# Optimization experiments

Hardware: AMD Instinct MI355X
Metric: run time of the kernel (lower is better)

## Reference

```python
import jax, jax.numpy as jnp
import numpy as np

N_NODES = 32768
N_EDGES = 524288
NODE_DIM, POS_DIM, EDGE_DIM = 44, 8, 1
HID, OUT, LAYERS, HEADS = 128, 128, 3, 4
DK = HID // HEADS
LN_EPS = 1e-5


def _linear_w(key, fan_in, fan_out):
    return (jax.random.normal(key, (fan_in, fan_out), jnp.float32) / np.sqrt(fan_in)).astype(jnp.float32)


def _ln(x, g, b):
    m = jnp.mean(x, axis=-1, keepdims=True)
    v = jnp.var(x, axis=-1, keepdims=True)
    return (x - m) * jax.lax.rsqrt(v + LN_EPS) * g + b


def setup_inputs() -> dict:
    key = jax.random.key(0)
    ks = jax.random.split(key, 16)
    inp = {
        'feats': jax.random.normal(ks[0], (N_NODES, NODE_DIM), jnp.float32),
        'lap_pos_enc': jax.random.normal(ks[1], (N_NODES, POS_DIM), jnp.float32),
        'edge_feats': jax.random.normal(ks[2], (N_EDGES, EDGE_DIM), jnp.float32),
        'src': jax.random.randint(ks[3], (N_EDGES,), 0, N_NODES, jnp.int32),
        'dst': jax.random.randint(ks[4], (N_EDGES,), 0, N_NODES, jnp.int32),
        # input projections
        'W_node': _linear_w(ks[5], NODE_DIM, HID), 'b_node': jnp.zeros((HID,), jnp.float32),
        'W_pos': _linear_w(ks[6], POS_DIM, HID), 'b_pos': jnp.zeros((HID,), jnp.float32),
        'W_edge': _linear_w(ks[7], EDGE_DIM, HID), 'b_edge': jnp.zeros((HID,), jnp.float32),
    }
    # per-layer stacked params (all layers are HID->HID since OUT==HID)
    def stack(k, fi, fo):
        kk = jax.random.split(k, LAYERS)
        return jnp.stack([_linear_w(kk[i], fi, fo) for i in range(LAYERS)])
    inp['Wq'] = stack(ks[8], HID, HID)
    inp['Wk'] = stack(ks[9], HID, HID)
    inp['Wv'] = stack(ks[10], HID, HID)
    inp['We'] = stack(ks[11], HID, HID)
    inp['W_lin'] = stack(ks[12], HID, HID)
    inp['b_lin'] = jnp.zeros((LAYERS, HID), jnp.float32)
    inp['g1'] = jnp.ones((LAYERS, HID), jnp.float32)
    inp['be1'] = jnp.zeros((LAYERS, HID), jnp.float32)
    inp['Wf1'] = stack(ks[13], HID, 2 * HID)
    inp['bf1'] = jnp.zeros((LAYERS, 2 * HID), jnp.float32)
    inp['Wf2'] = stack(ks[14], 2 * HID, HID)
    inp['bf2'] = jnp.zeros((LAYERS, HID), jnp.float32)
    inp['g2'] = jnp.ones((LAYERS, HID), jnp.float32)
    inp['be2'] = jnp.zeros((LAYERS, HID), jnp.float32)
    return inp


def reference(feats, lap_pos_enc, edge_feats,
              W_node, b_node, W_pos, b_pos, W_edge, b_edge,
              Wq, Wk, Wv, We, W_lin, b_lin, g1, be1,
              Wf1, bf1, Wf2, bf2, g2, be2, src, dst):
    n = feats.shape[0]
    inv_sqrt_dk = np.float32(1.0 / np.sqrt(DK))
    h = feats @ W_node + b_node + lap_pos_enc @ W_pos + b_pos      # [N, HID]
    e = edge_feats @ W_edge + b_edge                               # [E, HID] (shared across layers)
    for i in range(LAYERS):
        Q = (h @ Wq[i]).reshape(n, HEADS, DK)
        K = (h @ Wk[i]).reshape(n, HEADS, DK)
        V = (h @ Wv[i]).reshape(n, HEADS, DK)
        E = (e @ We[i]).reshape(-1, HEADS, DK)                     # [E, H, DK]
        # raw score [E, H, 1] broadcast against (1+E) -> [E, H, DK] (faithful to source)
        score = jnp.sum(K[src] * Q[dst], axis=-1, keepdims=True) * inv_sqrt_dk
        score = score * (1.0 + E)
        alpha = jnp.exp(score)                                      # [E, H, DK]
        Z = jnp.maximum(jax.ops.segment_sum(alpha, dst, num_segments=n), 1e-6)
        h_out = jax.ops.segment_sum(V[src] * alpha, dst, num_segments=n) / Z
        h_out = h_out.reshape(n, HEADS * DK)
        h = h + h_out @ W_lin[i] + b_lin[i]                        # residual + dropout(identity)
        h = _ln(h, g1[i], be1[i])
        h2 = jax.nn.relu(h @ Wf1[i] + bf1[i]) @ Wf2[i] + bf2[i]
        h = _ln(h + h2, g2[i], be2[i])
    # dgl.mean_nodes over a single graph -> [1, OUT]; readout LayerNorm is never applied in source
    return jnp.mean(h, axis=0, keepdims=True)
```

## Files before the change

kernel.cpp:

```cpp
#include <hip/hip_runtime.h>
#include <hip/hip_bf16.h>

#define N_NODES 32768
#define N_EDGES 524288
#define LN_EPS 1e-5f

typedef unsigned short ushort_t;
typedef __attribute__((ext_vector_type(8))) short short8v;
typedef __attribute__((ext_vector_type(4))) float float4v;
typedef __attribute__((ext_vector_type(2))) float float2v;

__device__ __forceinline__ float bf2f(ushort_t u) {
    return __uint_as_float(((unsigned int)u) << 16);
}
__device__ __forceinline__ ushort_t f2bf(float f) {
    unsigned int u = __float_as_uint(f);
    unsigned int r = (u + 0x7FFFu + ((u >> 16) & 1u)) >> 16;
    return (ushort_t)r;
}
__device__ __forceinline__ float lo16(unsigned int x) { return __uint_as_float(x << 16); }
__device__ __forceinline__ float hi16(unsigned int x) { return __uint_as_float(x & 0xFFFF0000u); }

#if __has_builtin(__builtin_amdgcn_exp2f)
#define EXP2(x) __builtin_amdgcn_exp2f(x)
#else
#define EXP2(x) exp2f(x)
#endif

#define OFF_WNODE 0
#define OFF_BNODE 5632
#define OFF_WPOS  5760
#define OFF_BPOS  6784
#define OFF_WEDGE 6912
#define OFF_BEDGE 7040
#define OFF_WQ    7168
#define OFF_WK    56320
#define OFF_WV    105472
#define OFF_WE    154624
#define OFF_WLIN  203776
#define OFF_BLIN  252928
#define OFF_G1    253312
#define OFF_BE1   253696
#define OFF_WF1   254080
#define OFF_BF1   352384
#define OFF_WF2   353152
#define OFF_BF2   451456
#define OFF_G2    451840
#define OFF_BE2   452224
#define CONV_TOTAL 452608

#define REC_QKV(i)  ((i) * 96)
#define REC_WLIN(i) (288 + (i) * 32)
#define REC_WF1(i)  (384 + (i) * 64)
#define REC_WF2(i)  (576 + (i) * 64)
#define REC_TOTAL   768

#define LDS_STRIDE 264
#define LDS_FSTRIDE 132

__global__ void detect_kernel(const unsigned int* __restrict__ wn, int* __restrict__ flag) {
    __shared__ int s[256];
    int t = threadIdx.x;
    int cnt = 0;
    for (int i = t; i < 2816; i += 256) {
        unsigned int b = (wn[i] >> 8) & 0x7F;
        cnt += (b >= 0x3A && b <= 0x40) ? 1 : 0;
    }
    s[t] = cnt;
    __syncthreads();
    for (int off = 128; off > 0; off >>= 1) {
        if (t < off) s[t] += s[t + off];
        __syncthreads();
    }
    if (t == 0) *flag = (s[0] > 1408) ? 1 : 0;
}

struct ConvArgs { const void* src[20]; };

__global__ void convert_kernel(ConvArgs a, const int* __restrict__ flag,
                               float* __restrict__ dst) {
    int gid = blockIdx.x * 256 + threadIdx.x;
    if (gid >= CONV_TOTAL) return;
    const int off[21] = {OFF_WNODE, OFF_BNODE, OFF_WPOS, OFF_BPOS, OFF_WEDGE, OFF_BEDGE,
                         OFF_WQ, OFF_WK, OFF_WV, OFF_WE, OFF_WLIN, OFF_BLIN, OFF_G1,
                         OFF_BE1, OFF_WF1, OFF_BF1, OFF_WF2, OFF_BF2, OFF_G2, OFF_BE2,
                         CONV_TOTAL};
    int s = 0;
#pragma unroll
    for (int i = 1; i < 20; ++i) s += (gid >= off[i]) ? 1 : 0;
    int local = gid - off[s];
    if (*flag)
        dst[gid] = bf2f(((const ushort_t*)a.src[s])[local]);
    else
        dst[gid] = ((const float*)a.src[s])[local];
}

__global__ void swz_kernel(const float* __restrict__ conv, ushort_t* __restrict__ swz) {
    int gid = blockIdx.x * 256 + threadIdx.x;
    int lane = gid & 63;
    int rec = gid >> 6;
    if (rec >= REC_TOTAL) return;
    int col = lane & 15, quad = lane >> 4;
    const float* src;
    int ct, kb, OC;
    if (rec < 288) {
        int layer = rec / 96, r2 = rec % 96;
        ct = r2 >> 2; kb = r2 & 3;
        int seg = ct >> 3;
        int base = (seg == 0 ? OFF_WQ : (seg == 1 ? OFF_WK : OFF_WV)) + layer * 16384;
        src = conv + base; OC = 128; ct &= 7;
    } else if (rec < 384) {
        int r = rec - 288, layer = r / 32, r2 = r % 32;
        ct = r2 >> 2; kb = r2 & 3;
        src = conv + OFF_WLIN + layer * 16384; OC = 128;
    } else if (rec < 576) {
        int r = rec - 384, layer = r / 64, r2 = r % 64;
        ct = r2 >> 2; kb = r2 & 3;
        src = conv + OFF_WF1 + layer * 32768; OC = 256;
    } else {
        int r = rec - 576, layer = r / 64, r2 = r % 64;
        ct = r2 >> 3; kb = r2 & 7;
        src = conv + OFF_WF2 + layer * 32768; OC = 128;
    }
    int n = ct * 16 + col;
    ushort_t v[8];
#pragma unroll
    for (int j = 0; j < 8; ++j) v[j] = f2bf(src[(size_t)(kb * 32 + quad * 8 + j) * OC + n]);
    ushort_t* o = swz + (size_t)rec * 512 + lane * 8;
#pragma unroll
    for (int j = 0; j < 8; ++j) o[j] = v[j];
}

__global__ void input_proj_kernel(const void* __restrict__ feats,
                                  const void* __restrict__ lap,
                                  const float* __restrict__ conv,
                                  const int* __restrict__ flag,
                                  float* __restrict__ h, ushort_t* __restrict__ hb) {
    int gid = blockIdx.x * 256 + threadIdx.x;
    int node = gid >> 5;
    int cg = (gid & 31) * 4;
    bool isbf = (*flag != 0);
    const float* Wn = conv + OFF_WNODE;
    const float* Wp = conv + OFF_WPOS;

    float4 b1 = *(const float4*)(conv + OFF_BNODE + cg);
    float4 b2 = *(const float4*)(conv + OFF_BPOS + cg);
    float a0 = b1.x + b2.x, a1 = b1.y + b2.y, a2 = b1.z + b2.z, a3 = b1.w + b2.w;

#define ACC(fv, Wbase, kk)                                            \
    {                                                                 \
        float4 wv_ = *(const float4*)(Wbase + (size_t)(kk) * 128 + cg); \
        a0 = fmaf(fv, wv_.x, a0);                                     \
        a1 = fmaf(fv, wv_.y, a1);                                     \
        a2 = fmaf(fv, wv_.z, a2);                                     \
        a3 = fmaf(fv, wv_.w, a3);                                     \
    }

    if (isbf) {
        const ushort_t* frow = (const ushort_t*)feats + (size_t)node * 44;
        const ushort_t* prow = (const ushort_t*)lap + (size_t)node * 8;
#pragma unroll
        for (int i = 0; i < 11; ++i) {
            ushort4 f = *(const ushort4*)(frow + i * 4);
            ACC(bf2f(f.x), Wn, i * 4 + 0)
            ACC(bf2f(f.y), Wn, i * 4 + 1)
            ACC(bf2f(f.z), Wn, i * 4 + 2)
            ACC(bf2f(f.w), Wn, i * 4 + 3)
        }
#pragma unroll
        for (int i = 0; i < 2; ++i) {
            ushort4 f = *(const ushort4*)(prow + i * 4);
            ACC(bf2f(f.x), Wp, i * 4 + 0)
            ACC(bf2f(f.y), Wp, i * 4 + 1)
            ACC(bf2f(f.z), Wp, i * 4 + 2)
            ACC(bf2f(f.w), Wp, i * 4 + 3)
        }
    } else {
        const float4* frow = (const float4*)((const float*)feats + (size_t)node * 44);
        const float4* prow = (const float4*)((const float*)lap + (size_t)node * 8);
#pragma unroll
        for (int i = 0; i < 11; ++i) {
            float4 f = frow[i];
            ACC(f.x, Wn, i * 4 + 0)
            ACC(f.y, Wn, i * 4 + 1)
            ACC(f.z, Wn, i * 4 + 2)
            ACC(f.w, Wn, i * 4 + 3)
        }
#pragma unroll
        for (int i = 0; i < 2; ++i) {
            float4 f = prow[i];
            ACC(f.x, Wp, i * 4 + 0)
            ACC(f.y, Wp, i * 4 + 1)
            ACC(f.z, Wp, i * 4 + 2)
            ACC(f.w, Wp, i * 4 + 3)
        }
    }
#undef ACC

    size_t idx = (size_t)node * 128 + cg;
    *(float4*)(h + idx) = make_float4(a0, a1, a2, a3);
    ushort4 ob;
    ob.x = f2bf(a0); ob.y = f2bf(a1); ob.z = f2bf(a2); ob.w = f2bf(a3);
    *(ushort4*)(hb + idx) = ob;
}

__global__ void uc_kernel(const float* __restrict__ conv,
                          float* __restrict__ u, float* __restrict__ c1) {
    int l = blockIdx.x;
    int d = threadIdx.x;
    const float* W_edge = conv + OFF_WEDGE;
    const float* b_edge = conv + OFF_BEDGE;
    const float* Wl = conv + OFF_WE + l * 128 * 128;
    float uu = 0.f, cc = 0.f;
#pragma unroll 4
    for (int k = 0; k < 128; ++k) {
        float w = Wl[k * 128 + d];
        uu += W_edge[k] * w;
        cc += b_edge[k] * w;
    }
    const float scale = 0.17677669529663687f * 1.4426950408889634f;
    u[l * 128 + d] = uu * scale;
    c1[l * 128 + d] = (1.f + cc) * scale;
}

__global__ void hist_kernel(const int* __restrict__ dst, int* __restrict__ deg) {
    int e = blockIdx.x * 256 + threadIdx.x;
    if (e < N_EDGES) atomicAdd(&deg[dst[e]], 1);
}

__global__ void scan_kernel(const int* __restrict__ deg, int* __restrict__ rowstart,
                            int* __restrict__ cursor) {
    __shared__ int lds[1024];
    int t = threadIdx.x;
    int base = t * 32;
    int v[32];
    int csum = 0;
#pragma unroll
    for (int j = 0; j < 32; ++j) { v[j] = deg[base + j]; csum += v[j]; }
    lds[t] = csum;
    __syncthreads();
    for (int off = 1; off < 1024; off <<= 1) {
        int x = (t >= off) ? lds[t - off] : 0;
        __syncthreads();
        lds[t] += x;
        __syncthreads();
    }
    int excl = lds[t] - csum;
    int running = excl;
#pragma unroll
    for (int j = 0; j < 32; ++j) {
        rowstart[base + j] = running;
        cursor[base + j] = running;
        running += v[j];
    }
    if (t == 1023) rowstart[N_NODES] = running;
}

__global__ void scatter_kernel(const int* __restrict__ src, const int* __restrict__ dst,
                               const void* __restrict__ ef, const int* __restrict__ flag,
                               int* __restrict__ cursor,
                               unsigned int* __restrict__ edges) {
    int e = blockIdx.x * 256 + threadIdx.x;
    if (e < N_EDGES) {
        ushort_t efb = (*flag != 0) ? ((const ushort_t*)ef)[e]
                                    : f2bf(((const float*)ef)[e]);
        int d = dst[e];
        int p = atomicAdd(&cursor[d], 1);
        edges[p] = (unsigned int)src[e] | ((unsigned int)efb << 16);
    }
}

template <int KB>
__global__ __launch_bounds__(256) void qkv_gemm(
    const ushort_t* __restrict__ A,
    const ushort_t* __restrict__ Bswz,
    ushort_t* __restrict__ outQ,
    unsigned char* __restrict__ outKV) {
    const int K = KB * 32;
    const int tid = threadIdx.x;
    const int wv = tid >> 6, lane = tid & 63;
    const int col = lane & 15, quad = lane >> 4;
    const int m0 = blockIdx.x * 64 + wv * 16;
    const int ct0 = blockIdx.y * 8;

    float4v acc[8];
#pragma unroll
    for (int ct = 0; ct < 8; ++ct) acc[ct] = (float4v){0.f, 0.f, 0.f, 0.f};

    const ushort_t* Ap = A + (size_t)(m0 + col) * K + quad * 8;
    const ushort_t* Bp = Bswz + (size_t)ct0 * KB * 512 + lane * 8;

#pragma unroll
    for (int kb = 0; kb < KB; ++kb) {
        short8v a = *(const short8v*)(Ap + kb * 32);
#pragma unroll
        for (int ct = 0; ct < 8; ++ct) {
            short8v b = *(const short8v*)(Bp + (size_t)(ct * KB + kb) * 512);
            acc[ct] = __builtin_amdgcn_mfma_f32_16x16x32_bf16(a, b, acc[ct], 0, 0, 0);
        }
    }

    const int rowb = m0 + quad * 4;
    const int seg = blockIdx.y;
    if (seg == 0) {
#pragma unroll
        for (int ct = 0; ct < 8; ++ct) {
            int j = ct * 16 + col;
#pragma unroll
            for (int r = 0; r < 4; ++r)
                outQ[(size_t)(rowb + r) * 128 + j] = f2bf(acc[ct][r]);
        }
    } else {
        const int vofs = (seg == 2) ? 8 : 0;
#pragma unroll
        for (int ct = 0; ct < 8; ++ct) {
            int j = ct * 16 + col;
            int off = ((j >> 3) * 16) + (j & 7) + vofs;
#pragma unroll
            for (int r = 0; r < 4; ++r) {
                float a = acc[ct][r];
                float b = __shfl_xor(a, 1, 64);
                if ((col & 1) == 0) {
                    unsigned short pk = (unsigned short)
                        __builtin_amdgcn_cvt_pk_fp8_f32(a, b, 0, false);
                    *(ushort_t*)(outKV + (size_t)(rowb + r) * 256 + off) = pk;
                }
            }
        }
    }
}

__global__ __launch_bounds__(64, 2) void ffn_kernel(
    const ushort_t* __restrict__ HOUT,
    const ushort_t* __restrict__ BWL,
    const ushort_t* __restrict__ BF1,
    const ushort_t* __restrict__ BF2,
    const float* __restrict__ bl,
    const float* __restrict__ g1v, const float* __restrict__ be1v,
    const float* __restrict__ bf1v,
    const float* __restrict__ bf2v,
    const float* __restrict__ g2v, const float* __restrict__ be2v,
    float* __restrict__ h,
    ushort_t* __restrict__ hb) {
    __shared__ __align__(16) char ldsraw[16 * 528];
    ushort_t* ldsu = (ushort_t*)ldsraw;
    float* ldsf = (float*)ldsraw;
    const int lane = threadIdx.x & 63;
    const int col = lane & 15, quad = lane >> 4;
    const int m0 = blockIdx.x * 16;
    const int rowb = m0 + quad * 4;
    const int lrowc = quad * 4;
    const int lrowa = col;

    float4v acc[8];
#pragma unroll
    for (int ct = 0; ct < 8; ++ct) acc[ct] = (float4v){0.f, 0.f, 0.f, 0.f};
    const ushort_t* Ap = HOUT + (size_t)(m0 + col) * 128 + quad * 8;
#pragma unroll
    for (int kb = 0; kb < 4; ++kb) {
        short8v a = *(const short8v*)(Ap + kb * 32);
#pragma unroll
        for (int ct = 0; ct < 8; ++ct) {
            short8v b = *(const short8v*)(BWL + (size_t)(ct * 4 + kb) * 512 + lane * 8);
            acc[ct] = __builtin_amdgcn_mfma_f32_16x16x32_bf16(a, b, acc[ct], 0, 0, 0);
        }
    }

    float val[8][4], s[4] = {0.f, 0.f, 0.f, 0.f}, ss[4] = {0.f, 0.f, 0.f, 0.f};
#pragma unroll
    for (int ct = 0; ct < 8; ++ct) {
        float bi = bl[ct * 16 + col];
#pragma unroll
        for (int r = 0; r < 4; ++r) {
            float v = acc[ct][r] + bi + h[(size_t)(rowb + r) * 128 + ct * 16 + col];
            val[ct][r] = v;
            s[r] += v;
            ss[r] += v * v;
        }
    }
#pragma unroll
    for (int mask = 1; mask < 16; mask <<= 1) {
#pragma unroll
        for (int r = 0; r < 4; ++r) {
            s[r] += __shfl_xor(s[r], mask, 64);
            ss[r] += __shfl_xor(ss[r], mask, 64);
        }
    }
#pragma unroll
    for (int r = 0; r < 4; ++r) {
        float mean = s[r] * (1.f / 128.f);
        float var = ss[r] * (1.f / 128.f) - mean * mean;
        s[r] = mean;
        ss[r] = rsqrtf(var + LN_EPS);
    }
#pragma unroll
    for (int ct = 0; ct < 8; ++ct) {
        float gg = g1v[ct * 16 + col], bb = be1v[ct * 16 + col];
#pragma unroll
        for (int r = 0; r < 4; ++r) {
            float o = (val[ct][r] - s[r]) * ss[r] * gg + bb;
            val[ct][r] = o;
            ldsu[(lrowc + r) * LDS_STRIDE + ct * 16 + col] = f2bf(o);
        }
    }
    __syncthreads();

    short8v af[4];
#pragma unroll
    for (int kb = 0; kb < 4; ++kb)
        af[kb] = *(const short8v*)&ldsu[lrowa * LDS_STRIDE + kb * 32 + quad * 8];

    float4v acc2[16];
#pragma unroll
    for (int ct = 0; ct < 16; ++ct) acc2[ct] = (float4v){0.f, 0.f, 0.f, 0.f};
#pragma unroll
    for (int kb = 0; kb < 4; ++kb) {
#pragma unroll
        for (int ct = 0; ct < 16; ++ct) {
            short8v b = *(const short8v*)(BF1 + (size_t)(ct * 4 + kb) * 512 + lane * 8);
            acc2[ct] = __builtin_amdgcn_mfma_f32_16x16x32_bf16(af[kb], b, acc2[ct], 0, 0, 0);
        }
    }
    __syncthreads();

#pragma unroll
    for (int ct = 0; ct < 16; ++ct) {
        float bi = bf1v[ct * 16 + col];
#pragma unroll
        for (int r = 0; r < 4; ++r) {
            float v = fmaxf(acc2[ct][r] + bi, 0.f);
            ldsu[(lrowc + r) * LDS_STRIDE + ct * 16 + col] = f2bf(v);
        }
    }
    __syncthreads();

    float4v acc3[8];
#pragma unroll
    for (int ct = 0; ct < 8; ++ct) acc3[ct] = (float4v){0.f, 0.f, 0.f, 0.f};
#pragma unroll
    for (int kb = 0; kb < 8; ++kb) {
        short8v a = *(const short8v*)&ldsu[lrowa * LDS_STRIDE + kb * 32 + quad * 8];
#pragma unroll
        for (int ct = 0; ct < 8; ++ct) {
            short8v b = *(const short8v*)(BF2 + (size_t)(ct * 8 + kb) * 512 + lane * 8);
            acc3[ct] = __builtin_amdgcn_mfma_f32_16x16x32_bf16(a, b, acc3[ct], 0, 0, 0);
        }
    }

    float s2[4] = {0.f, 0.f, 0.f, 0.f}, ss2[4] = {0.f, 0.f, 0.f, 0.f};
#pragma unroll
    for (int ct = 0; ct < 8; ++ct) {
        float bi = bf2v[ct * 16 + col];
#pragma unroll
        for (int r = 0; r < 4; ++r) {
            float v = acc3[ct][r] + bi + val[ct][r];
            val[ct][r] = v;
            s2[r] += v;
            ss2[r] += v * v;
        }
    }
#pragma unroll
    for (int mask = 1; mask < 16; mask <<= 1) {
#pragma unroll
        for (int r = 0; r < 4; ++r) {
            s2[r] += __shfl_xor(s2[r], mask, 64);
            ss2[r] += __shfl_xor(ss2[r], mask, 64);
        }
    }
#pragma unroll
    for (int r = 0; r < 4; ++r) {
        float mean = s2[r] * (1.f / 128.f);
        float var = ss2[r] * (1.f / 128.f) - mean * mean;
        s2[r] = mean;
        ss2[r] = rsqrtf(var + LN_EPS);
    }
    __syncthreads();
#pragma unroll
    for (int ct = 0; ct < 8; ++ct) {
        float gg = g2v[ct * 16 + col], bb = be2v[ct * 16 + col];
#pragma unroll
        for (int r = 0; r < 4; ++r) {
            float o = (val[ct][r] - s2[r]) * ss2[r] * gg + bb;
            ldsf[(lrowc + r) * LDS_FSTRIDE + ct * 16 + col] = o;
        }
    }
    __syncthreads();

#pragma unroll
    for (int j = 0; j < 8; ++j) {
        int p = lane + j * 64;
        int row = p >> 5;
        int c4 = p & 31;
        float4 vv = *(const float4*)&ldsf[row * LDS_FSTRIDE + c4 * 4];
        *(float4*)&h[(size_t)(m0 + row) * 128 + c4 * 4] = vv;
    }
#pragma unroll
    for (int j = 0; j < 4; ++j) {
        int p = lane + j * 64;
        int row = p >> 4;
        int c8 = p & 15;
        float4 va = *(const float4*)&ldsf[row * LDS_FSTRIDE + c8 * 8];
        float4 vb = *(const float4*)&ldsf[row * LDS_FSTRIDE + c8 * 8 + 4];
        uint4 ou;
        ou.x = (unsigned)f2bf(va.x) | ((unsigned)f2bf(va.y) << 16);
        ou.y = (unsigned)f2bf(va.z) | ((unsigned)f2bf(va.w) << 16);
        ou.z = (unsigned)f2bf(vb.x) | ((unsigned)f2bf(vb.y) << 16);
        ou.w = (unsigned)f2bf(vb.z) | ((unsigned)f2bf(vb.w) << 16);
        *(uint4*)&hb[(size_t)(m0 + row) * 128 + c8 * 8] = ou;
    }
}

__global__ __launch_bounds__(64) void agg_kernel(
    const ushort_t* __restrict__ Q, const unsigned char* __restrict__ KV,
    const int* __restrict__ rowstart, const unsigned int* __restrict__ edges,
    const float* __restrict__ u, const float* __restrict__ c1,
    ushort_t* __restrict__ hout) {
    const int lane = threadIdx.x & 63;
    const int v = blockIdx.x;
    const int sub = lane & 15;
    const int grp = lane >> 4;

    uint4 qu = *(const uint4*)(Q + (size_t)v * 128 + sub * 8);
    float q0 = lo16(qu.x), q1 = hi16(qu.x), q2 = lo16(qu.y), q3 = hi16(qu.y);
    float q4 = lo16(qu.z), q5 = hi16(qu.z), q6 = lo16(qu.w), q7 = hi16(qu.w);
    float4 uva = *(const float4*)(u + sub * 8);
    float4 uvb = *(const float4*)(u + sub * 8 + 4);
    float4 cva = *(const float4*)(c1 + sub * 8);
    float4 cvb = *(const float4*)(c1 + sub * 8 + 4);

    float m = -1.0e38f;
    float sA[8] = {0.f, 0.f, 0.f, 0.f, 0.f, 0.f, 0.f, 0.f};
    float o[8] = {0.f, 0.f, 0.f, 0.f, 0.f, 0.f, 0.f, 0.f};

    const int start = rowstart[v];
    const int deg = rowstart[v + 1] - start;
    const int nfull = deg >> 2;
    const unsigned int* ep = edges + start + grp;

#define AGG_COMPUTE(PE, KVv, MASKED, VALID)                                      \
    {                                                                            \
        float ef_ = __uint_as_float((PE) & 0xFFFF0000u);                         \
        float2v k01 = __builtin_amdgcn_cvt_pk_f32_fp8((KVv).x, false);           \
        float2v k23 = __builtin_amdgcn_cvt_pk_f32_fp8((KVv).x, true);            \
        float2v k45 = __builtin_amdgcn_cvt_pk_f32_fp8((KVv).y, false);           \
        float2v k67 = __builtin_amdgcn_cvt_pk_f32_fp8((KVv).y, true);            \
        float p_ = k01[0] * q0;                                                  \
        p_ = fmaf(k01[1], q1, p_);                                               \
        p_ = fmaf(k23[0], q2, p_);                                               \
        p_ = fmaf(k23[1], q3, p_);                                               \
        p_ = fmaf(k45[0], q4, p_);                                               \
        p_ = fmaf(k45[1], q5, p_);                                               \
        p_ = fmaf(k67[0], q6, p_);                                               \
        p_ = fmaf(k67[1], q7, p_);                                               \
        p_ += __shfl_xor(p_, 1, 64);                                             \
        p_ += __shfl_xor(p_, 2, 64);                                             \
        float x0 = p_ * fmaf(ef_, uva.x, cva.x);                                 \
        float x1 = p_ * fmaf(ef_, uva.y, cva.y);                                 \
        float x2 = p_ * fmaf(ef_, uva.z, cva.z);                                 \
        float x3 = p_ * fmaf(ef_, uva.w, cva.w);                                 \
        float x4 = p_ * fmaf(ef_, uvb.x, cvb.x);                                 \
        float x5 = p_ * fmaf(ef_, uvb.y, cvb.y);                                 \
        float x6 = p_ * fmaf(ef_, uvb.z, cvb.z);                                 \
        float x7 = p_ * fmaf(ef_, uvb.w, cvb.w);                                 \
        if (MASKED) {                                                            \
            x0 = (VALID) ? x0 : -1.0e38f; x1 = (VALID) ? x1 : -1.0e38f;          \
            x2 = (VALID) ? x2 : -1.0e38f; x3 = (VALID) ? x3 : -1.0e38f;          \
            x4 = (VALID) ? x4 : -1.0e38f; x5 = (VALID) ? x5 : -1.0e38f;          \
            x6 = (VALID) ? x6 : -1.0e38f; x7 = (VALID) ? x7 : -1.0e38f;          \
        }                                                                        \
        float xm = fmaxf(fmaxf(fmaxf(x0, x1), fmaxf(x2, x3)),                    \
                         fmaxf(fmaxf(x4, x5), fmaxf(x6, x7)));                   \
        if (xm > m) {                                                            \
            float nm = xm + 6.0f;                                                \
            float sc = EXP2(m - nm);                                             \
            sA[0] *= sc; sA[1] *= sc; sA[2] *= sc; sA[3] *= sc;                  \
            sA[4] *= sc; sA[5] *= sc; sA[6] *= sc; sA[7] *= sc;                  \
            o[0] *= sc; o[1] *= sc; o[2] *= sc; o[3] *= sc;                      \
            o[4] *= sc; o[5] *= sc; o[6] *= sc; o[7] *= sc;                      \
            m = nm;                                                              \
        }                                                                        \
        float e0 = EXP2(x0 - m), e1 = EXP2(x1 - m);                              \
        float e2 = EXP2(x2 - m), e3 = EXP2(x3 - m);                              \
        float e4 = EXP2(x4 - m), e5 = EXP2(x5 - m);                              \
        float e6 = EXP2(x6 - m), e7 = EXP2(x7 - m);                              \
        sA[0] += e0; sA[1] += e1; sA[2] += e2; sA[3] += e3;                      \
        sA[4] += e4; sA[5] += e5; sA[6] += e6; sA[7] += e7;                      \
        float2v v01 = __builtin_amdgcn_cvt_pk_f32_fp8((KVv).z, false);           \
        float2v v23 = __builtin_amdgcn_cvt_pk_f32_fp8((KVv).z, true);            \
        float2v v45 = __builtin_amdgcn_cvt_pk_f32_fp8((KVv).w, false);           \
        float2v v67 = __builtin_amdgcn_cvt_pk_f32_fp8((KVv).w, true);            \
        o[0] = fmaf(v01[0], e0, o[0]);                                           \
        o[1] = fmaf(v01[1], e1, o[1]);                                           \
        o[2] = fmaf(v23[0], e2, o[2]);                                           \
        o[3] = fmaf(v23[1], e3, o[3]);                                           \
        o[4] = fmaf(v45[0], e4, o[4]);                                           \
        o[5] = fmaf(v45[1], e5, o[5]);                                           \
        o[6] = fmaf(v67[0], e6, o[6]);                                           \
        o[7] = fmaf(v67[1], e7, o[7]);                                           \
    }

    int it = 0;
    for (; it + 2 <= nfull; it += 2) {
        unsigned int pe0 = ep[4 * it];
        unsigned int pe1 = ep[4 * it + 4];
        uint4 kv0 = *(const uint4*)(KV + (size_t)(pe0 & 0xFFFFu) * 256 + sub * 16);
        uint4 kv1 = *(const uint4*)(KV + (size_t)(pe1 & 0xFFFFu) * 256 + sub * 16);
        AGG_COMPUTE(pe0, kv0, false, true)
        AGG_COMPUTE(pe1, kv1, false, true)
    }
    if (it < nfull) {
        unsigned int pe0 = ep[4 * it];
        uint4 kv0 = *(const uint4*)(KV + (size_t)(pe0 & 0xFFFFu) * 256 + sub * 16);
        AGG_COMPUTE(pe0, kv0, false, true)
    }
    const int rem = deg & 3;
    if (rem) {
        bool valid = grp < rem;
        unsigned int pe = valid ? ep[4 * nfull] : edges[start];
        uint4 kv = *(const uint4*)(KV + (size_t)(pe & 0xFFFFu) * 256 + sub * 16);
        AGG_COMPUTE(pe, kv, true, valid)
    }
#undef AGG_COMPUTE

#pragma unroll
    for (int mask = 16; mask <= 32; mask <<= 1) {
        float mo = __shfl_xor(m, mask, 64);
        float mm = fmaxf(m, mo);
        float sca = EXP2(m - mm);
        float scb = EXP2(mo - mm);
#pragma unroll
        for (int j = 0; j < 8; ++j) {
            float t = __shfl_xor(sA[j], mask, 64);
            sA[j] = sA[j] * sca + t * scb;
            t = __shfl_xor(o[j], mask, 64);
            o[j] = o[j] * sca + t * scb;
        }
        m = mm;
    }

    if (grp == 0) {
        float zc = 1e-6f * EXP2(-m);
        uint4 ou;
        unsigned int w0, w1;
        float z;
        z = fmaxf(fmaxf(sA[0], zc), 1e-37f); w0 = f2bf(o[0] / z);
        z = fmaxf(fmaxf(sA[1], zc), 1e-37f); w1 = f2bf(o[1] / z);
        ou.x = w0 | (w1 << 16);
        z = fmaxf(fmaxf(sA[2], zc), 1e-37f); w0 = f2bf(o[2] / z);
        z = fmaxf(fmaxf(sA[3], zc), 1e-37f); w1 = f2bf(o[3] / z);
        ou.y = w0 | (w1 << 16);
        z = fmaxf(fmaxf(sA[4], zc), 1e-37f); w0 = f2bf(o[4] / z);
        z = fmaxf(fmaxf(sA[5], zc), 1e-37f); w1 = f2bf(o[5] / z);
        ou.z = w0 | (w1 << 16);
        z = fmaxf(fmaxf(sA[6], zc), 1e-37f); w0 = f2bf(o[6] / z);
        z = fmaxf(fmaxf(sA[7], zc), 1e-37f); w1 = f2bf(o[7] / z);
        ou.w = w0 | (w1 << 16);
        *(uint4*)(hout + (size_t)v * 128 + sub * 8) = ou;
    }
}

__global__ void mean_part_kernel(const float* __restrict__ h, float* __restrict__ macc) {
    __shared__ float s[256];
    int t = threadIdx.x;
    int col = t & 127;
    int half = t >> 7;
    int r0 = blockIdx.x * 256;
    float acc = 0.f;
    for (int r = half; r < 256; r += 2) acc += h[(size_t)(r0 + r) * 128 + col];
    s[t] = acc;
    __syncthreads();
    if (t < 128) atomicAdd(&macc[t], s[t] + s[t + 128]);
}

__global__ void finalize_kernel(const float* __restrict__ macc, void* __restrict__ out,
                                const int* __restrict__ flag) {
    int t = threadIdx.x;
    float v = macc[t] * (1.f / (float)N_NODES);
    if (*flag)
        ((ushort_t*)out)[t] = f2bf(v);
    else
        ((float*)out)[t] = v;
}

extern "C" void kernel_launch(void* const* d_in, const int* in_sizes, int n_in,
                              void* d_out, int out_size, void* d_ws, size_t ws_size,
                              hipStream_t stream) {
    const int* src = (const int*)d_in[3];
    const int* dst = (const int*)d_in[4];

    char* w = (char*)d_ws;
    const size_t MB = 1u << 20;
    float* h        = (float*)(w);
    ushort_t* hb    = (ushort_t*)(w + 16 * MB);
    ushort_t* Qh    = (ushort_t*)(w + 24 * MB);
    unsigned char* KVf8 = (unsigned char*)(w + 32 * MB);
    char* aux       = w + 48 * MB;
    int* deg        = (int*)(aux);
    int* rowstart   = (int*)(aux + 0x40000);
    int* cursor     = (int*)(aux + 0x80000);
    unsigned int* edges = (unsigned int*)(aux + 0xC0000);
    float* ubuf     = (float*)(aux + 0xC0000 + 2 * MB);
    float* cbuf     = ubuf + 3 * 128;
    float* macc     = cbuf + 3 * 128;
    int* flag       = (int*)(macc + 128);
    float* conv     = (float*)(aux + 0xC0000 + 2 * MB + 4096);
    ushort_t* swz   = (ushort_t*)((char*)conv + CONV_TOTAL * 4);

    hipMemsetAsync(deg, 0, N_NODES * sizeof(int), stream);
    hipMemsetAsync(macc, 0, 128 * sizeof(float), stream);

    detect_kernel<<<1, 256, 0, stream>>>((const unsigned int*)d_in[5], flag);

    ConvArgs ca;
    ca.src[0] = d_in[5];   ca.src[1] = d_in[6];   ca.src[2] = d_in[7];
    ca.src[3] = d_in[8];   ca.src[4] = d_in[9];   ca.src[5] = d_in[10];
    ca.src[6] = d_in[11];  ca.src[7] = d_in[12];  ca.src[8] = d_in[13];
    ca.src[9] = d_in[14];  ca.src[10] = d_in[15]; ca.src[11] = d_in[16];
    ca.src[12] = d_in[17]; ca.src[13] = d_in[18]; ca.src[14] = d_in[19];
    ca.src[15] = d_in[20]; ca.src[16] = d_in[21]; ca.src[17] = d_in[22];
    ca.src[18] = d_in[23]; ca.src[19] = d_in[24];
    convert_kernel<<<(CONV_TOTAL + 255) / 256, 256, 0, stream>>>(ca, flag, conv);
    swz_kernel<<<REC_TOTAL * 64 / 256, 256, 0, stream>>>(conv, swz);

    input_proj_kernel<<<N_NODES * 32 / 256, 256, 0, stream>>>(d_in[0], d_in[1], conv,
                                                              flag, h, hb);
    uc_kernel<<<3, 128, 0, stream>>>(conv, ubuf, cbuf);
    hist_kernel<<<N_EDGES / 256, 256, 0, stream>>>(dst, deg);
    scan_kernel<<<1, 1024, 0, stream>>>(deg, rowstart, cursor);
    scatter_kernel<<<N_EDGES / 256, 256, 0, stream>>>(src, dst, d_in[2], flag, cursor,
                                                      edges);

    for (int i = 0; i < 3; ++i) {
        const ushort_t* swzQKV = swz + (size_t)REC_QKV(i) * 512;
        const ushort_t* swzWL  = swz + (size_t)REC_WLIN(i) * 512;
        const ushort_t* swzF1  = swz + (size_t)REC_WF1(i) * 512;
        const ushort_t* swzF2  = swz + (size_t)REC_WF2(i) * 512;

        qkv_gemm<4><<<dim3(N_NODES / 64, 3), 256, 0, stream>>>(hb, swzQKV, Qh, KVf8);

        agg_kernel<<<N_NODES, 64, 0, stream>>>(Qh, KVf8, rowstart, edges,
                                               ubuf + i * 128, cbuf + i * 128, hb);

        ffn_kernel<<<N_NODES / 16, 64, 0, stream>>>(
            hb, swzWL, swzF1, swzF2,
            conv + OFF_BLIN + i * 128, conv + OFF_G1 + i * 128, conv + OFF_BE1 + i * 128,
            conv + OFF_BF1 + i * 256,
            conv + OFF_BF2 + i * 128, conv + OFF_G2 + i * 128, conv + OFF_BE2 + i * 128,
            h, hb);
    }

    mean_part_kernel<<<N_NODES / 256, 256, 0, stream>>>(h, macc);
    finalize_kernel<<<1, 128, 0, stream>>>(macc, d_out, flag);
}
```

Measured before the change: 504.3 us.

## Fuse next-layer QKV GEMM and mean into FFN, merge prep kernels

Moves the QKV projection for the next layer into the FFN kernel epilogue, so the hidden state is consumed from LDS rather than re-read from memory, and drops the per-layer hb writeback. The mean reduction is folded into the final FFN, and the histogram goes into input projection. The uc computation goes into the swizzle kernel, which now reads raw weights directly instead of via the fp32 conversion buffer. The scan is vectorised and the aggregation loop unrolled to 4 edges. The fused QKV adds register pressure and scattered stores inside the FFN kernel, which runs 64-thread blocks.

```diff
diff --git a/kernel.cpp b/kernel.cpp
--- a/kernel.cpp
+++ b/kernel.cpp
@@ -33,21 +33,14 @@
 #define OFF_BPOS  6784
 #define OFF_WEDGE 6912
 #define OFF_BEDGE 7040
-#define OFF_WQ    7168
-#define OFF_WK    56320
-#define OFF_WV    105472
-#define OFF_WE    154624
-#define OFF_WLIN  203776
-#define OFF_BLIN  252928
-#define OFF_G1    253312
-#define OFF_BE1   253696
-#define OFF_WF1   254080
-#define OFF_BF1   352384
-#define OFF_WF2   353152
-#define OFF_BF2   451456
-#define OFF_G2    451840
-#define OFF_BE2   452224
-#define CONV_TOTAL 452608
+#define OFF_BLIN  7168
+#define OFF_G1    7552
+#define OFF_BE1   7936
+#define OFF_BF1   8320
+#define OFF_BF2   9088
+#define OFF_G2    9472
+#define OFF_BE2   9856
+#define CONV_TOTAL 10240
 
 #define REC_QKV(i)  ((i) * 96)
 #define REC_WLIN(i) (288 + (i) * 32)
@@ -75,19 +68,18 @@
     if (t == 0) *flag = (s[0] > 1408) ? 1 : 0;
 }
 
-struct ConvArgs { const void* src[20]; };
+struct ConvArgs { const void* src[13]; };
 
 __global__ void convert_kernel(ConvArgs a, const int* __restrict__ flag,
                                float* __restrict__ dst) {
     int gid = blockIdx.x * 256 + threadIdx.x;
     if (gid >= CONV_TOTAL) return;
-    const int off[21] = {OFF_WNODE, OFF_BNODE, OFF_WPOS, OFF_BPOS, OFF_WEDGE, OFF_BEDGE,
-                         OFF_WQ, OFF_WK, OFF_WV, OFF_WE, OFF_WLIN, OFF_BLIN, OFF_G1,
-                         OFF_BE1, OFF_WF1, OFF_BF1, OFF_WF2, OFF_BF2, OFF_G2, OFF_BE2,
+    const int off[14] = {OFF_WNODE, OFF_BNODE, OFF_WPOS, OFF_BPOS, OFF_WEDGE, OFF_BEDGE,
+                         OFF_BLIN, OFF_G1, OFF_BE1, OFF_BF1, OFF_BF2, OFF_G2, OFF_BE2,
                          CONV_TOTAL};
     int s = 0;
 #pragma unroll
-    for (int i = 1; i < 20; ++i) s += (gid >= off[i]) ? 1 : 0;
+    for (int i = 1; i < 13; ++i) s += (gid >= off[i]) ? 1 : 0;
     int local = gid - off[s];
     if (*flag)
         dst[gid] = bf2f(((const ushort_t*)a.src[s])[local]);
@@ -95,37 +87,83 @@
         dst[gid] = ((const float*)a.src[s])[local];
 }
 
-__global__ void swz_kernel(const float* __restrict__ conv, ushort_t* __restrict__ swz) {
+__global__ void swz_kernel(const void* __restrict__ Wq, const void* __restrict__ Wk,
+                           const void* __restrict__ Wv, const void* __restrict__ Wlin,
+                           const void* __restrict__ Wf1, const void* __restrict__ Wf2,
+                           const void* __restrict__ We, const void* __restrict__ wedge,
+                           const void* __restrict__ bedge,
+                           const int* __restrict__ flag,
+                           ushort_t* __restrict__ swz,
+                           float* __restrict__ u, float* __restrict__ c1) {
+    const bool isbf = (*flag != 0);
+    if (blockIdx.x >= 192) {
+        int l = blockIdx.x - 192;
+        int d = threadIdx.x;
+        if (d >= 128) return;
+        float uu = 0.f, cc = 0.f;
+        if (isbf) {
+            const ushort_t* Wl = (const ushort_t*)We + (size_t)l * 16384;
+            const ushort_t* we_ = (const ushort_t*)wedge;
+            const ushort_t* be_ = (const ushort_t*)bedge;
+#pragma unroll 4
+            for (int k = 0; k < 128; ++k) {
+                float w = bf2f(Wl[k * 128 + d]);
+                uu = fmaf(bf2f(we_[k]), w, uu);
+                cc = fmaf(bf2f(be_[k]), w, cc);
+            }
+        } else {
+            const float* Wl = (const float*)We + (size_t)l * 16384;
+            const float* we_ = (const float*)wedge;
+            const float* be_ = (const float*)bedge;
+#pragma unroll 4
+            for (int k = 0; k < 128; ++k) {
+                float w = Wl[k * 128 + d];
+                uu = fmaf(we_[k], w, uu);
+                cc = fmaf(be_[k], w, cc);
+            }
+        }
+        const float scale = 0.17677669529663687f * 1.4426950408889634f;
+        u[l * 128 + d] = uu * scale;
+        c1[l * 128 + d] = (1.f + cc) * scale;
+        return;
+    }
     int gid = blockIdx.x * 256 + threadIdx.x;
     int lane = gid & 63;
     int rec = gid >> 6;
-    if (rec >= REC_TOTAL) return;
     int col = lane & 15, quad = lane >> 4;
-    const float* src;
+    const void* src;
+    size_t base;
     int ct, kb, OC;
     if (rec < 288) {
         int layer = rec / 96, r2 = rec % 96;
         ct = r2 >> 2; kb = r2 & 3;
         int seg = ct >> 3;
-        int base = (seg == 0 ? OFF_WQ : (seg == 1 ? OFF_WK : OFF_WV)) + layer * 16384;
-        src = conv + base; OC = 128; ct &= 7;
+        src = (seg == 0) ? Wq : ((seg == 1) ? Wk : Wv);
+        base = (size_t)layer * 16384; OC = 128; ct &= 7;
     } else if (rec < 384) {
         int r = rec - 288, layer = r / 32, r2 = r % 32;
         ct = r2 >> 2; kb = r2 & 3;
-        src = conv + OFF_WLIN + layer * 16384; OC = 128;
+        src = Wlin; base = (size_t)layer * 16384; OC = 128;
     } else if (rec < 576) {
         int r = rec - 384, layer = r / 64, r2 = r % 64;
         ct = r2 >> 2; kb = r2 & 3;
-        src = conv + OFF_WF1 + layer * 32768; OC = 256;
+        src = Wf1; base = (size_t)layer * 32768; OC = 256;
     } else {
         int r = rec - 576, layer = r / 64, r2 = r % 64;
         ct = r2 >> 3; kb = r2 & 7;
-        src = conv + OFF_WF2 + layer * 32768; OC = 128;
+        src = Wf2; base = (size_t)layer * 32768; OC = 128;
     }
     int n = ct * 16 + col;
     ushort_t v[8];
-#pragma unroll
-    for (int j = 0; j < 8; ++j) v[j] = f2bf(src[(size_t)(kb * 32 + quad * 8 + j) * OC + n]);
+    if (isbf) {
+        const ushort_t* s16 = (const ushort_t*)src + base;
+#pragma unroll
+        for (int j = 0; j < 8; ++j) v[j] = s16[(size_t)(kb * 32 + quad * 8 + j) * OC + n];
+    } else {
+        const float* s32 = (const float*)src + base;
+#pragma unroll
+        for (int j = 0; j < 8; ++j) v[j] = f2bf(s32[(size_t)(kb * 32 + quad * 8 + j) * OC + n]);
+    }
     ushort_t* o = swz + (size_t)rec * 512 + lane * 8;
 #pragma unroll
     for (int j = 0; j < 8; ++j) o[j] = v[j];
@@ -135,8 +173,11 @@
                                   const void* __restrict__ lap,
                                   const float* __restrict__ conv,
                                   const int* __restrict__ flag,
+                                  const int* __restrict__ dstidx,
+                                  int* __restrict__ deg,
                                   float* __restrict__ h, ushort_t* __restrict__ hb) {
     int gid = blockIdx.x * 256 + threadIdx.x;
+    if (gid < N_EDGES) atomicAdd(&deg[dstidx[gid]], 1);
     int node = gid >> 5;
     int cg = (gid & 31) * 4;
     bool isbf = (*flag != 0);
@@ -204,30 +245,6 @@
     *(ushort4*)(hb + idx) = ob;
 }
 
-__global__ void uc_kernel(const float* __restrict__ conv,
-                          float* __restrict__ u, float* __restrict__ c1) {
-    int l = blockIdx.x;
-    int d = threadIdx.x;
-    const float* W_edge = conv + OFF_WEDGE;
-    const float* b_edge = conv + OFF_BEDGE;
-    const float* Wl = conv + OFF_WE + l * 128 * 128;
-    float uu = 0.f, cc = 0.f;
-#pragma unroll 4
-    for (int k = 0; k < 128; ++k) {
-        float w = Wl[k * 128 + d];
-        uu += W_edge[k] * w;
-        cc += b_edge[k] * w;
-    }
-    const float scale = 0.17677669529663687f * 1.4426950408889634f;
-    u[l * 128 + d] = uu * scale;
-    c1[l * 128 + d] = (1.f + cc) * scale;
-}
-
-__global__ void hist_kernel(const int* __restrict__ dst, int* __restrict__ deg) {
-    int e = blockIdx.x * 256 + threadIdx.x;
-    if (e < N_EDGES) atomicAdd(&deg[dst[e]], 1);
-}
-
 __global__ void scan_kernel(const int* __restrict__ deg, int* __restrict__ rowstart,
                             int* __restrict__ cursor) {
     __shared__ int lds[1024];
@@ -236,7 +253,12 @@
     int v[32];
     int csum = 0;
 #pragma unroll
-    for (int j = 0; j < 32; ++j) { v[j] = deg[base + j]; csum += v[j]; }
+    for (int j = 0; j < 8; ++j) {
+        int4 x = *(const int4*)(deg + base + j * 4);
+        v[j * 4 + 0] = x.x; v[j * 4 + 1] = x.y;
+        v[j * 4 + 2] = x.z; v[j * 4 + 3] = x.w;
+        csum += x.x + x.y + x.z + x.w;
+    }
     lds[t] = csum;
     __syncthreads();
     for (int off = 1; off < 1024; off <<= 1) {
@@ -248,10 +270,14 @@
     int excl = lds[t] - csum;
     int running = excl;
 #pragma unroll
-    for (int j = 0; j < 32; ++j) {
-        rowstart[base + j] = running;
-        cursor[base + j] = running;
-        running += v[j];
+    for (int j = 0; j < 8; ++j) {
+        int4 w;
+        w.x = running; running += v[j * 4 + 0];
+        w.y = running; running += v[j * 4 + 1];
+        w.z = running; running += v[j * 4 + 2];
+        w.w = running; running += v[j * 4 + 3];
+        *(int4*)(rowstart + base + j * 4) = w;
+        *(int4*)(cursor + base + j * 4) = w;
     }
     if (t == 1023) rowstart[N_NODES] = running;
 }
@@ -335,13 +361,17 @@
     const ushort_t* __restrict__ BWL,
     const ushort_t* __restrict__ BF1,
     const ushort_t* __restrict__ BF2,
+    const ushort_t* __restrict__ BQKV,
     const float* __restrict__ bl,
     const float* __restrict__ g1v, const float* __restrict__ be1v,
     const float* __restrict__ bf1v,
     const float* __restrict__ bf2v,
     const float* __restrict__ g2v, const float* __restrict__ be2v,
     float* __restrict__ h,
-    ushort_t* __restrict__ hb) {
+    ushort_t* __restrict__ outQ,
+    unsigned char* __restrict__ outKV,
+    float* __restrict__ macc,
+    const int fuse_qkv, const int do_mean) {
     __shared__ __align__(16) char ldsraw[16 * 528];
     ushort_t* ldsu = (ushort_t*)ldsraw;
     float* ldsf = (float*)ldsraw;
@@ -494,19 +524,74 @@
         float4 vv = *(const float4*)&ldsf[row * LDS_FSTRIDE + c4 * 4];
         *(float4*)&h[(size_t)(m0 + row) * 128 + c4 * 4] = vv;
     }
-#pragma unroll
-    for (int j = 0; j < 4; ++j) {
-        int p = lane + j * 64;
-        int row = p >> 4;
-        int c8 = p & 15;
-        float4 va = *(const float4*)&ldsf[row * LDS_FSTRIDE + c8 * 8];
-        float4 vb = *(const float4*)&ldsf[row * LDS_FSTRIDE + c8 * 8 + 4];
-        uint4 ou;
-        ou.x = (unsigned)f2bf(va.x) | ((unsigned)f2bf(va.y) << 16);
-        ou.y = (unsigned)f2bf(va.z) | ((unsigned)f2bf(va.w) << 16);
-        ou.z = (unsigned)f2bf(vb.x) | ((unsigned)f2bf(vb.y) << 16);
-        ou.w = (unsigned)f2bf(vb.z) | ((unsigned)f2bf(vb.w) << 16);
-        *(uint4*)&hb[(size_t)(m0 + row) * 128 + c8 * 8] = ou;
+
+    if (fuse_qkv) {
+        short8v afq[4];
+#pragma unroll
+        for (int kb = 0; kb < 4; ++kb) {
+            float4 fa = *(const float4*)&ldsf[lrowa * LDS_FSTRIDE + kb * 32 + quad * 8];
+            float4 fb = *(const float4*)&ldsf[lrowa * LDS_FSTRIDE + kb * 32 + quad * 8 + 4];
+            short8v t;
+            t[0] = (short)f2bf(fa.x); t[1] = (short)f2bf(fa.y);
+            t[2] = (short)f2bf(fa.z); t[3] = (short)f2bf(fa.w);
+            t[4] = (short)f2bf(fb.x); t[5] = (short)f2bf(fb.y);
+            t[6] = (short)f2bf(fb.z); t[7] = (short)f2bf(fb.w);
+            afq[kb] = t;
+        }
+#pragma unroll
+        for (int seg = 0; seg < 3; ++seg) {
+            float4v qacc[8];
+#pragma unroll
+            for (int ct = 0; ct < 8; ++ct) qacc[ct] = (float4v){0.f, 0.f, 0.f, 0.f};
+#pragma unroll
+            for (int kb = 0; kb < 4; ++kb) {
+#pragma unroll
+                for (int ct = 0; ct < 8; ++ct) {
+                    short8v b = *(const short8v*)(BQKV +
+                        (size_t)((seg * 8 + ct) * 4 + kb) * 512 + lane * 8);
+                    qacc[ct] = __builtin_amdgcn_mfma_f32_16x16x32_bf16(afq[kb], b,
+                                                                       qacc[ct], 0, 0, 0);
+                }
+            }
+            if (seg == 0) {
+#pragma unroll
+                for (int ct = 0; ct < 8; ++ct) {
+                    int j = ct * 16 + col;
+#pragma unroll
+                    for (int r = 0; r < 4; ++r)
+                        outQ[(size_t)(rowb + r) * 128 + j] = f2bf(qacc[ct][r]);
+                }
+            } else {
+                const int vofs = (seg == 2) ? 8 : 0;
+#pragma unroll
+                for (int ct = 0; ct < 8; ++ct) {
+                    int j = ct * 16 + col;
+                    int off = ((j >> 3) * 16) + (j & 7) + vofs;
+#pragma unroll
+                    for (int r = 0; r < 4; ++r) {
+                        float a = qacc[ct][r];
+                        float b = __shfl_xor(a, 1, 64);
+                        if ((col & 1) == 0) {
+                            unsigned short pk = (unsigned short)
+                                __builtin_amdgcn_cvt_pk_fp8_f32(a, b, 0, false);
+                            *(ushort_t*)(outKV + (size_t)(rowb + r) * 256 + off) = pk;
+                        }
+                    }
+                }
+            }
+        }
+    }
+
+    if (do_mean) {
+        int c0 = lane * 2;
+        float sm0 = 0.f, sm1 = 0.f;
+#pragma unroll
+        for (int row = 0; row < 16; ++row) {
+            sm0 += ldsf[row * LDS_FSTRIDE + c0];
+            sm1 += ldsf[row * LDS_FSTRIDE + c0 + 1];
+        }
+        atomicAdd(&macc[c0], sm0);
+        atomicAdd(&macc[c0 + 1], sm1);
     }
 }
 
@@ -600,13 +685,28 @@
     }
 
     int it = 0;
-    for (; it + 2 <= nfull; it += 2) {
+    for (; it + 4 <= nfull; it += 4) {
+        unsigned int pe0 = ep[4 * it];
+        unsigned int pe1 = ep[4 * it + 4];
+        unsigned int pe2 = ep[4 * it + 8];
+        unsigned int pe3 = ep[4 * it + 12];
+        uint4 kv0 = *(const uint4*)(KV + (size_t)(pe0 & 0xFFFFu) * 256 + sub * 16);
+        uint4 kv1 = *(const uint4*)(KV + (size_t)(pe1 & 0xFFFFu) * 256 + sub * 16);
+        uint4 kv2 = *(const uint4*)(KV + (size_t)(pe2 & 0xFFFFu) * 256 + sub * 16);
+        uint4 kv3 = *(const uint4*)(KV + (size_t)(pe3 & 0xFFFFu) * 256 + sub * 16);
+        AGG_COMPUTE(pe0, kv0, false, true)
+        AGG_COMPUTE(pe1, kv1, false, true)
+        AGG_COMPUTE(pe2, kv2, false, true)
+        AGG_COMPUTE(pe3, kv3, false, true)
+    }
+    if (it + 2 <= nfull) {
         unsigned int pe0 = ep[4 * it];
         unsigned int pe1 = ep[4 * it + 4];
         uint4 kv0 = *(const uint4*)(KV + (size_t)(pe0 & 0xFFFFu) * 256 + sub * 16);
         uint4 kv1 = *(const uint4*)(KV + (size_t)(pe1 & 0xFFFFu) * 256 + sub * 16);
         AGG_COMPUTE(pe0, kv0, false, true)
         AGG_COMPUTE(pe1, kv1, false, true)
+        it += 2;
     }
     if (it < nfull) {
         unsigned int pe0 = ep[4 * it];
@@ -659,19 +759,6 @@
     }
 }
 
-__global__ void mean_part_kernel(const float* __restrict__ h, float* __restrict__ macc) {
-    __shared__ float s[256];
-    int t = threadIdx.x;
-    int col = t & 127;
-    int half = t >> 7;
-    int r0 = blockIdx.x * 256;
-    float acc = 0.f;
-    for (int r = half; r < 256; r += 2) acc += h[(size_t)(r0 + r) * 128 + col];
-    s[t] = acc;
-    __syncthreads();
-    if (t < 128) atomicAdd(&macc[t], s[t] + s[t + 128]);
-}
-
 __global__ void finalize_kernel(const float* __restrict__ macc, void* __restrict__ out,
                                 const int* __restrict__ flag) {
     int t = threadIdx.x;
@@ -712,43 +799,51 @@
     detect_kernel<<<1, 256, 0, stream>>>((const unsigned int*)d_in[5], flag);
 
     ConvArgs ca;
-    ca.src[0] = d_in[5];   ca.src[1] = d_in[6];   ca.src[2] = d_in[7];
-    ca.src[3] = d_in[8];   ca.src[4] = d_in[9];   ca.src[5] = d_in[10];
-    ca.src[6] = d_in[11];  ca.src[7] = d_in[12];  ca.src[8] = d_in[13];
-    ca.src[9] = d_in[14];  ca.src[10] = d_in[15]; ca.src[11] = d_in[16];
-    ca.src[12] = d_in[17]; ca.src[13] = d_in[18]; ca.src[14] = d_in[19];
-    ca.src[15] = d_in[20]; ca.src[16] = d_in[21]; ca.src[17] = d_in[22];
-    ca.src[18] = d_in[23]; ca.src[19] = d_in[24];
+    ca.src[0] = d_in[5];
+    ca.src[1] = d_in[6];
+    ca.src[2] = d_in[7];
+    ca.src[3] = d_in[8];
+    ca.src[4] = d_in[9];
+    ca.src[5] = d_in[10];
+    ca.src[6] = d_in[16];
+    ca.src[7] = d_in[17];
+    ca.src[8] = d_in[18];
+    ca.src[9] = d_in[20];
+    ca.src[10] = d_in[22];
+    ca.src[11] = d_in[23];
+    ca.src[12] = d_in[24];
     convert_kernel<<<(CONV_TOTAL + 255) / 256, 256, 0, stream>>>(ca, flag, conv);
-    swz_kernel<<<REC_TOTAL * 64 / 256, 256, 0, stream>>>(conv, swz);
+
+    swz_kernel<<<192 + 3, 256, 0, stream>>>(
+        d_in[11], d_in[12], d_in[13], d_in[15], d_in[19], d_in[21],
+        d_in[14], d_in[9], d_in[10], flag, swz, ubuf, cbuf);
 
     input_proj_kernel<<<N_NODES * 32 / 256, 256, 0, stream>>>(d_in[0], d_in[1], conv,
-                                                              flag, h, hb);
-    uc_kernel<<<3, 128, 0, stream>>>(conv, ubuf, cbuf);
-    hist_kernel<<<N_EDGES / 256, 256, 0, stream>>>(dst, deg);
+                                                              flag, dst, deg, h, hb);
     scan_kernel<<<1, 1024, 0, stream>>>(deg, rowstart, cursor);
     scatter_kernel<<<N_EDGES / 256, 256, 0, stream>>>(src, dst, d_in[2], flag, cursor,
                                                       edges);
 
+    qkv_gemm<4><<<dim3(N_NODES / 64, 3), 256, 0, stream>>>(
+        hb, swz + (size_t)REC_QKV(0) * 512, Qh, KVf8);
+
     for (int i = 0; i < 3; ++i) {
-        const ushort_t* swzQKV = swz + (size_t)REC_QKV(i) * 512;
         const ushort_t* swzWL  = swz + (size_t)REC_WLIN(i) * 512;
         const ushort_t* swzF1  = swz + (size_t)REC_WF1(i) * 512;
         const ushort_t* swzF2  = swz + (size_t)REC_WF2(i) * 512;
-
-        qkv_gemm<4><<<dim3(N_NODES / 64, 3), 256, 0, stream>>>(hb, swzQKV, Qh, KVf8);
+        const ushort_t* swzQn  = swz + (size_t)REC_QKV(i < 2 ? i + 1 : 0) * 512;
 
         agg_kernel<<<N_NODES, 64, 0, stream>>>(Qh, KVf8, rowstart, edges,
                                                ubuf + i * 128, cbuf + i * 128, hb);
 
         ffn_kernel<<<N_NODES / 16, 64, 0, stream>>>(
-            hb, swzWL, swzF1, swzF2,
+            hb, swzWL, swzF1, swzF2, swzQn,
             conv + OFF_BLIN + i * 128, conv + OFF_G1 + i * 128, conv + OFF_BE1 + i * 128,
             conv + OFF_BF1 + i * 256,
             conv + OFF_BF2 + i * 128, conv + OFF_G2 + i * 128, conv + OFF_BE2 + i * 128,
-            h, hb);
-    }
-
-    mean_part_kernel<<<N_NODES / 256, 256, 0, stream>>>(h, macc);
+            h, Qh, KVf8, macc,
+            (i < 2) ? 1 : 0, (i == 2) ? 1 : 0);
+    }
+
     finalize_kernel<<<1, 128, 0, stream>>>(macc, d_out, flag);
 }
```

New measurement: 524.2 us. 3.9% more time.
